# Performance work log

Hardware: AMD Instinct MI355X
Metric: run time of the kernel (lower is better)

## Reference

```python
import jax, jax.numpy as jnp
import numpy as np


def setup_inputs() -> dict:
    key = jax.random.key(0)
    k1, k2, k3 = jax.random.split(key, 3)
    bs, r, d = 4, 4096, 64
    G = jax.random.uniform(k1, (bs, d), dtype=jnp.float32)          # eigenvalues (non-negative)
    V = jax.random.normal(k2, (bs, r, d), dtype=jnp.float32)        # eigenvectors / spectral embedding
    weights = jax.random.uniform(k3, (1,), dtype=jnp.float32)       # learned scalar t
    return {"G": G, "V": V, "weights": weights}


def reference(G, V, weights):
    # Original: eVs = diag(max(G,0)^(2t)); y = E@eVs@Phi2^T + Phi2@eVs@E^T - 2*Phi@eVs@Phi^T
    # Since eVs is diagonal, this is the weighted pairwise squared distance:
    # y[b,i,j] = sum_k w[b,k] * (V[b,i,k] - V[b,j,k])^2 with w = max(G,0)^(2t).
    t = weights[0]
    w = jnp.maximum(G, jnp.zeros_like(G)) ** (2.0 * t)   # (bs, d)
    Vw = V * w[:, None, :]                               # (bs, r, d) elementwise diag scaling
    s = jnp.sum(Vw * V, axis=-1)                         # (bs, r): weighted squared norms
    cross = jnp.einsum('brd,bsd->brs', Vw, V)            # (bs, r, r)
    y = s[:, :, None] + s[:, None, :] - 2.0 * cross
    return y
```

## Files before the change

### kernel.cpp

```cpp
#include <hip/hip_runtime.h>
#include <hip/hip_bf16.h>


typedef __attribute__((ext_vector_type(8))) short bf16x8;
typedef __attribute__((ext_vector_type(4))) float f32x4;

constexpr int BS = 4, R = 4096, D = 64;
constexpr int LS = 260;

__global__ __launch_bounds__(256) void prep_kernel(
    const float* __restrict__ G, const float* __restrict__ V,
    const float* __restrict__ wt,
    __hip_bfloat16* __restrict__ vw_bf, __hip_bfloat16* __restrict__ v_bf,
    float* __restrict__ s)
{
    int row  = blockIdx.x * 4 + (threadIdx.x >> 6);
    int lane = threadIdx.x & 63;
    if (row >= BS * R) return;
    int b = row / R;

    float t2 = 2.0f * wt[0];
    float g  = fmaxf(G[b * D + lane], 0.0f);
    float w  = powf(g, t2);
    float v  = V[(size_t)row * D + lane];

    __hip_bfloat16 vb  = __float2bfloat16(v);
    __hip_bfloat16 vwb = __float2bfloat16(w * v);
    v_bf [(size_t)row * D + lane] = vb;
    vw_bf[(size_t)row * D + lane] = vwb;

    float prod = __bfloat162float(vwb) * __bfloat162float(vb);
    #pragma unroll
    for (int off = 32; off; off >>= 1) prod += __shfl_down(prod, off);
    if (lane == 0) s[row] = prod;
}

__global__ __launch_bounds__(512) void dist_kernel(
    const short* __restrict__ vw_bf, const short* __restrict__ v_bf,
    const float* __restrict__ s, float* __restrict__ out)
{
    __shared__ float lds[64 * LS];

    int lane = threadIdx.x & 63;
    int wave = threadIdx.x >> 6;
    int wr   = wave >> 2;
    int wc   = wave & 3;

    int b  = blockIdx.z;
    int jb = blockIdx.x * 256;
    int i0 = blockIdx.y * 128;

    const short* A  = vw_bf + ((size_t)b * R + i0 + wr * 64) * D;
    const short* B  = v_bf  + ((size_t)b * R + jb + wc * 64) * D;
    const float* sb = s + (size_t)b * R;

    int lrow = lane & 15;
    int kgrp = lane >> 4;

    bf16x8 a[4][2];
    #pragma unroll
    for (int rb = 0; rb < 4; ++rb)
        #pragma unroll
        for (int ks = 0; ks < 2; ++ks)
            a[rb][ks] = *(const bf16x8*)(A + (rb * 16 + lrow) * D + ks * 32 + kgrp * 8);

    f32x4 acc[4][4];
    #pragma unroll
    for (int rb = 0; rb < 4; ++rb)
        #pragma unroll
        for (int jt = 0; jt < 4; ++jt)
            acc[rb][jt] = f32x4{0.f, 0.f, 0.f, 0.f};

    #pragma unroll
    for (int jt = 0; jt < 4; ++jt) {
        const short* Bt = B + jt * 16 * D;
        bf16x8 b0 = *(const bf16x8*)(Bt + lrow * D +      kgrp * 8);
        bf16x8 b1 = *(const bf16x8*)(Bt + lrow * D + 32 + kgrp * 8);
        #pragma unroll
        for (int rb = 0; rb < 4; ++rb) {
            acc[rb][jt] = __builtin_amdgcn_mfma_f32_16x16x32_bf16(a[rb][0], b0, acc[rb][jt], 0, 0, 0);
            acc[rb][jt] = __builtin_amdgcn_mfma_f32_16x16x32_bf16(a[rb][1], b1, acc[rb][jt], 0, 0, 0);
        }
    }

    float si_lane = sb[i0 + wr * 64 + lane];

    float* outb = out + ((size_t)b * R + i0) * R + jb;

    #pragma unroll
    for (int c = 0; c < 2; ++c) {
        if (wr == c) {
            #pragma unroll
            for (int rb = 0; rb < 4; ++rb) {
                #pragma unroll
                for (int rg = 0; rg < 4; ++rg) {
                    int rl = rb * 16 + kgrp * 4 + rg;
                    float si = __shfl(si_lane, rl);
                    #pragma unroll
                    for (int jt = 0; jt < 4; ++jt) {
                        float sj = sb[jb + wc * 64 + jt * 16 + lrow];
                        float y  = si + sj - 2.0f * acc[rb][jt][rg];
                        lds[rl * LS + wc * 64 + jt * 16 + lrow] = y;
                    }
                }
            }
        }
        __syncthreads();

        #pragma unroll
        for (int r = 0; r < 8; ++r) {
            int rl = wave * 8 + r;
            f32x4 v = *(const f32x4*)&lds[rl * LS + lane * 4];
            __builtin_nontemporal_store(v,
                (f32x4*)(outb + (size_t)(c * 64 + rl) * R + lane * 4));
        }
        if (c == 0) __syncthreads();
    }
}

extern "C" void kernel_launch(void* const* d_in, const int* in_sizes, int n_in,
                              void* d_out, int out_size, void* d_ws, size_t ws_size,
                              hipStream_t stream) {
    const float* G  = (const float*)d_in[0];
    const float* V  = (const float*)d_in[1];
    const float* wt = (const float*)d_in[2];
    float* out = (float*)d_out;

    char* ws = (char*)d_ws;
    __hip_bfloat16* vw_bf = (__hip_bfloat16*)ws;
    __hip_bfloat16* v_bf  = (__hip_bfloat16*)(ws + (size_t)BS * R * D * 2);
    float*          s     = (float*)        (ws + (size_t)BS * R * D * 4);

    prep_kernel<<<BS * R / 4, 256, 0, stream>>>(G, V, wt, vw_bf, v_bf, s);

    dim3 grid(R / 256, R / 128, BS);
    dist_kernel<<<grid, 512, 0, stream>>>((const short*)vw_bf, (const short*)v_bf,
                                          s, out);
}
```

Measured before the change: 66.72 us.

## Use symmetric sqrt-weighted embedding and enlarge output tile to 256x256

Prep now computes a single bf16 array u = g^t * V so the cross term becomes U·U^T and the squared norms are |u|^2, halving the prepared operand data and writes. The distance kernel tile grows to 256x256 per block with each wave computing 64x128, doubling accumulator registers and LDS staging size. This cuts redundant operand loads and halves the block count, at the cost of higher register and LDS use that lowers occupancy for a store-bound kernel.

```diff
diff --git a/kernel.cpp b/kernel.cpp
--- a/kernel.cpp
+++ b/kernel.cpp
@@ -11,47 +11,45 @@
 __global__ __launch_bounds__(256) void prep_kernel(
     const float* __restrict__ G, const float* __restrict__ V,
     const float* __restrict__ wt,
-    __hip_bfloat16* __restrict__ vw_bf, __hip_bfloat16* __restrict__ v_bf,
-    float* __restrict__ s)
+    __hip_bfloat16* __restrict__ u_bf, float* __restrict__ s)
 {
     int row  = blockIdx.x * 4 + (threadIdx.x >> 6);
     int lane = threadIdx.x & 63;
     if (row >= BS * R) return;
     int b = row / R;
 
-    float t2 = 2.0f * wt[0];
+    float t  = wt[0];
     float g  = fmaxf(G[b * D + lane], 0.0f);
-    float w  = powf(g, t2);
-    float v  = V[(size_t)row * D + lane];
+    float sw = powf(g, t);
+    float u  = sw * V[(size_t)row * D + lane];
 
-    __hip_bfloat16 vb  = __float2bfloat16(v);
-    __hip_bfloat16 vwb = __float2bfloat16(w * v);
-    v_bf [(size_t)row * D + lane] = vb;
-    vw_bf[(size_t)row * D + lane] = vwb;
+    __hip_bfloat16 ub = __float2bfloat16(u);
+    u_bf[(size_t)row * D + lane] = ub;
 
-    float prod = __bfloat162float(vwb) * __bfloat162float(vb);
+    float uf   = __bfloat162float(ub);
+    float prod = uf * uf;
     #pragma unroll
     for (int off = 32; off; off >>= 1) prod += __shfl_down(prod, off);
     if (lane == 0) s[row] = prod;
 }
 
 __global__ __launch_bounds__(512) void dist_kernel(
-    const short* __restrict__ vw_bf, const short* __restrict__ v_bf,
-    const float* __restrict__ s, float* __restrict__ out)
+    const short* __restrict__ U, const float* __restrict__ s,
+    float* __restrict__ out)
 {
-    __shared__ float lds[64 * LS];
+    __shared__ float lds[128 * LS];
 
     int lane = threadIdx.x & 63;
     int wave = threadIdx.x >> 6;
-    int wr   = wave >> 2;
-    int wc   = wave & 3;
+    int wr   = wave >> 1;
+    int wc   = wave & 1;
 
     int b  = blockIdx.z;
     int jb = blockIdx.x * 256;
-    int i0 = blockIdx.y * 128;
+    int i0 = blockIdx.y * 256;
 
-    const short* A  = vw_bf + ((size_t)b * R + i0 + wr * 64) * D;
-    const short* B  = v_bf  + ((size_t)b * R + jb + wc * 64) * D;
+    const short* Ap = U + ((size_t)b * R + i0 + wr * 64) * D;
+    const short* Bp = U + ((size_t)b * R + jb + wc * 128) * D;
     const float* sb = s + (size_t)b * R;
 
     int lrow = lane & 15;
@@ -62,18 +60,18 @@
     for (int rb = 0; rb < 4; ++rb)
         #pragma unroll
         for (int ks = 0; ks < 2; ++ks)
-            a[rb][ks] = *(const bf16x8*)(A + (rb * 16 + lrow) * D + ks * 32 + kgrp * 8);
+            a[rb][ks] = *(const bf16x8*)(Ap + (rb * 16 + lrow) * D + ks * 32 + kgrp * 8);
 
-    f32x4 acc[4][4];
+    f32x4 acc[4][8];
     #pragma unroll
     for (int rb = 0; rb < 4; ++rb)
         #pragma unroll
-        for (int jt = 0; jt < 4; ++jt)
+        for (int jt = 0; jt < 8; ++jt)
             acc[rb][jt] = f32x4{0.f, 0.f, 0.f, 0.f};
 
     #pragma unroll
-    for (int jt = 0; jt < 4; ++jt) {
-        const short* Bt = B + jt * 16 * D;
+    for (int jt = 0; jt < 8; ++jt) {
+        const short* Bt = Bp + jt * 16 * D;
         bf16x8 b0 = *(const bf16x8*)(Bt + lrow * D +      kgrp * 8);
         bf16x8 b1 = *(const bf16x8*)(Bt + lrow * D + 32 + kgrp * 8);
         #pragma unroll
@@ -84,12 +82,16 @@
     }
 
     float si_lane = sb[i0 + wr * 64 + lane];
+    float sj[8];
+    #pragma unroll
+    for (int jt = 0; jt < 8; ++jt) sj[jt] = sb[jb + wc * 128 + jt * 16 + lrow];
 
     float* outb = out + ((size_t)b * R + i0) * R + jb;
 
     #pragma unroll
     for (int c = 0; c < 2; ++c) {
-        if (wr == c) {
+        if ((wr >> 1) == c) {
+            int rbase = (wr & 1) * 64;
             #pragma unroll
             for (int rb = 0; rb < 4; ++rb) {
                 #pragma unroll
@@ -97,10 +99,9 @@
                     int rl = rb * 16 + kgrp * 4 + rg;
                     float si = __shfl(si_lane, rl);
                     #pragma unroll
-                    for (int jt = 0; jt < 4; ++jt) {
-                        float sj = sb[jb + wc * 64 + jt * 16 + lrow];
-                        float y  = si + sj - 2.0f * acc[rb][jt][rg];
-                        lds[rl * LS + wc * 64 + jt * 16 + lrow] = y;
+                    for (int jt = 0; jt < 8; ++jt) {
+                        float y = si + sj[jt] - 2.0f * acc[rb][jt][rg];
+                        lds[(rbase + rl) * LS + wc * 128 + jt * 16 + lrow] = y;
                     }
                 }
             }
@@ -108,11 +109,11 @@
         __syncthreads();
 
         #pragma unroll
-        for (int r = 0; r < 8; ++r) {
-            int rl = wave * 8 + r;
+        for (int r = 0; r < 16; ++r) {
+            int rl = wave * 16 + r;
             f32x4 v = *(const f32x4*)&lds[rl * LS + lane * 4];
             __builtin_nontemporal_store(v,
-                (f32x4*)(outb + (size_t)(c * 64 + rl) * R + lane * 4));
+                (f32x4*)(outb + (size_t)(c * 128 + rl) * R + lane * 4));
         }
         if (c == 0) __syncthreads();
     }
@@ -127,13 +128,11 @@
     float* out = (float*)d_out;
 
     char* ws = (char*)d_ws;
-    __hip_bfloat16* vw_bf = (__hip_bfloat16*)ws;
-    __hip_bfloat16* v_bf  = (__hip_bfloat16*)(ws + (size_t)BS * R * D * 2);
-    float*          s     = (float*)        (ws + (size_t)BS * R * D * 4);
+    __hip_bfloat16* u_bf = (__hip_bfloat16*)ws;
+    float*          s    = (float*)        (ws + (size_t)BS * R * D * 2);
 
-    prep_kernel<<<BS * R / 4, 256, 0, stream>>>(G, V, wt, vw_bf, v_bf, s);
+    prep_kernel<<<BS * R / 4, 256, 0, stream>>>(G, V, wt, u_bf, s);
 
-    dim3 grid(R / 256, R / 128, BS);
-    dist_kernel<<<grid, 512, 0, stream>>>((const short*)vw_bf, (const short*)v_bf,
-                                          s, out);
+    dim3 grid(R / 256, R / 256, BS);
+    dist_kernel<<<grid, 512, 0, stream>>>((const short*)u_bf, s, out);
 }
```

Measured after the change: 73.48 us. +10.1%, slower.
